# Performance work log

Hardware: AMD Instinct MI355X
Metric: run time of the kernel (lower is better)

## Reference

```python
import jax, jax.numpy as jnp
import numpy as np

N_NODES = 50000
N_EDGES = 800000
N_GRAPHS = 256
IN_CH = 128
HID = 256
FFN = 256
OUT = 1


def xavier(key, shape):
    fan_in, fan_out = shape[0], shape[1]
    a = jnp.sqrt(6.0 / (fan_in + fan_out))
    return jax.random.uniform(key, shape, jnp.float32, -a, a)


def setup_inputs() -> dict:
    key = jax.random.key(0)
    ks = jax.random.split(key, 12)
    x = jax.random.normal(ks[0], (N_NODES, IN_CH), jnp.float32)
    edge_index = jax.random.randint(ks[1], (2, N_EDGES), 0, N_NODES, jnp.int32)
    batch = jnp.sort(jax.random.randint(ks[2], (N_NODES,), 0, N_GRAPHS, jnp.int32))
    return {
        "x": x,
        "edge_index": edge_index,
        "batch": batch,
        # GCNConv layers (glorot weight, zero bias as in PyG reset_parameters)
        "W1": xavier(ks[3], (IN_CH, HID)), "b1": jnp.zeros((HID,), jnp.float32),
        "W2": xavier(ks[4], (HID, HID)),   "b2": jnp.zeros((HID,), jnp.float32),
        "W3": xavier(ks[5], (HID, HID)),   "b3": jnp.zeros((HID,), jnp.float32),
        # FFN: Linear(HID, FFN) then final Linear(FFN, OUT)
        "Wf": xavier(ks[6], (HID, FFN)),   "bf": jnp.zeros((FFN,), jnp.float32),
        "Wo": xavier(ks[7], (FFN, OUT)),   "bo": jnp.zeros((OUT,), jnp.float32),
    }


def _gcn_norm(edge_index, n_nodes):
    # add self-loops, compute symmetric normalization D^-1/2 (A+I) D^-1/2
    loops = jnp.arange(n_nodes, dtype=edge_index.dtype)
    row = jnp.concatenate([edge_index[0], loops])
    col = jnp.concatenate([edge_index[1], loops])
    deg = jax.ops.segment_sum(jnp.ones_like(col, jnp.float32), col, num_segments=n_nodes)
    dis = jnp.where(deg > 0, jax.lax.rsqrt(jnp.maximum(deg, 1.0)), 0.0)
    norm = dis[row] * dis[col]  # [E+N]
    return row, col, norm


def _gcn_conv(x, W, b, row, col, norm, n_nodes):
    xw = x @ W                                   # [N, H]
    msg = xw[row] * norm[:, None]                # gather + scale  [E+N, H]
    out = jax.ops.segment_sum(msg, col, num_segments=n_nodes)
    return out + b


def reference(x, edge_index, batch, W1, b1, W2, b2, W3, b3, Wf, bf, Wo, bo):
    row, col, norm = _gcn_norm(edge_index, N_NODES)
    h = jax.nn.relu(_gcn_conv(x, W1, b1, row, col, norm, N_NODES))
    h = jax.nn.relu(_gcn_conv(h, W2, b2, row, col, norm, N_NODES))
    h = jax.nn.relu(_gcn_conv(h, W3, b3, row, col, norm, N_NODES))
    # global mean pool over graphs
    counts = jax.ops.segment_sum(jnp.ones((N_NODES,), jnp.float32), batch, num_segments=N_GRAPHS)
    pooled = jax.ops.segment_sum(h, batch, num_segments=N_GRAPHS) / jnp.maximum(counts, 1.0)[:, None]
    # FFN (dropout is identity in eval mode): Linear -> ReLU -> final Linear
    g = jax.nn.relu(pooled @ Wf + bf)
    out = g @ Wo + bo
    return out
```

## Files before the change

### kernel.cpp

```cpp
#include <hip/hip_runtime.h>
#include <hip/hip_bf16.h>
#include <hip/hip_fp16.h>


#define THREADS 256
#define EPB 2048

typedef _Float16 f16x8 __attribute__((ext_vector_type(8)));
typedef float    f32x4 __attribute__((ext_vector_type(4)));
typedef unsigned short u16x8 __attribute__((ext_vector_type(8)));


__global__ void degree_goff_kernel(const int* __restrict__ col, int* __restrict__ deg, int E,
                                   const int* __restrict__ batch, int* __restrict__ goff,
                                   int N, int G) {
    int i = blockIdx.x * THREADS + threadIdx.x;
    if (i < E) atomicAdd(&deg[col[i]], 1);
    if (i < N) {
        int b1 = batch[i];
        int b0 = (i == 0) ? -1 : batch[i - 1];
        for (int g = b0 + 1; g <= b1; ++g) goff[g] = i;
        if (i == N - 1) {
            for (int g = b1 + 1; g <= G; ++g) goff[g] = N;
        }
    }
}

__global__ void bucketcnt_kernel(const int* __restrict__ deg, const int* __restrict__ batch,
                                 int* __restrict__ bcnt, int N) {
    int i = blockIdx.x * THREADS + threadIdx.x;
    if (i < N) {
        int key = (batch[i] << 3) | min((deg[i] + 7) >> 3, 7);
        atomicAdd(&bcnt[key], 1);
    }
}

__global__ __launch_bounds__(256) void bucketscan_kernel(int* __restrict__ b) {
    __shared__ int wsum[4];
    int t = threadIdx.x, lane = t & 63, wid = t >> 6;
    int base = t * 8;
    int v[8];
    #pragma unroll
    for (int k = 0; k < 8; ++k) v[k] = b[base + k];
    int s = 0;
    #pragma unroll
    for (int k = 0; k < 8; ++k) s += v[k];
    int inc = s;
    #pragma unroll
    for (int d = 1; d < 64; d <<= 1) {
        int u = __shfl_up(inc, d);
        if (lane >= d) inc += u;
    }
    if (lane == 63) wsum[wid] = inc;
    __syncthreads();
    int add = 0;
    for (int w = 0; w < wid; ++w) add += wsum[w];
    int ex = add + inc - s;
    #pragma unroll
    for (int k = 0; k < 8; ++k) { int t2 = v[k]; b[base + k] = ex; ex += t2; }
}

__global__ void place_kernel(const int* __restrict__ deg, const int* __restrict__ batch,
                             int* __restrict__ bcnt, int* __restrict__ perm,
                             int* __restrict__ pinv, int* __restrict__ batch_p, int N) {
    int i = blockIdx.x * THREADS + threadIdx.x;
    if (i < N) {
        int g = batch[i];
        int key = (g << 3) | min((deg[i] + 7) >> 3, 7);
        int pos = atomicAdd(&bcnt[key], 1);
        perm[pos] = i; pinv[i] = pos; batch_p[pos] = g;
    }
}

__global__ void translate_kernel(const int* __restrict__ row, const int* __restrict__ col,
                                 const int* __restrict__ pinv,
                                 unsigned short* __restrict__ rowp,
                                 unsigned short* __restrict__ colp, int E) {
    int e0 = (blockIdx.x * THREADS + threadIdx.x) * 8;
    if (e0 >= E) return;
    if (e0 + 8 <= E) {
        int4 c0 = *(const int4*)&col[e0];
        int4 c1 = *(const int4*)&col[e0 + 4];
        int4 r0 = *(const int4*)&row[e0];
        int4 r1 = *(const int4*)&row[e0 + 4];
        int cs[8] = {c0.x, c0.y, c0.z, c0.w, c1.x, c1.y, c1.z, c1.w};
        int rs[8] = {r0.x, r0.y, r0.z, r0.w, r1.x, r1.y, r1.z, r1.w};
        u16x8 cp, rp;
        #pragma unroll
        for (int j = 0; j < 8; ++j) {
            cp[j] = (unsigned short)pinv[cs[j]];
            rp[j] = (unsigned short)pinv[rs[j]];
        }
        *(u16x8*)&colp[e0] = cp;
        *(u16x8*)&rowp[e0] = rp;
    } else {
        for (int j = 0; j < 8 && e0 + j < E; ++j) {
            colp[e0 + j] = (unsigned short)pinv[col[e0 + j]];
            rowp[e0 + j] = (unsigned short)pinv[row[e0 + j]];
        }
    }
}

__global__ __launch_bounds__(256) void scanA_kernel(
    const int* __restrict__ deg, const int* __restrict__ perm,
    int* __restrict__ out, int* __restrict__ bsum,
    float* __restrict__ dis, int* __restrict__ degp, int n) {
    __shared__ int wsum[4];
    int i0 = blockIdx.x * 1024 + threadIdx.x * 4;
    int lane = threadIdx.x & 63, wid = threadIdx.x >> 6;
    int v0 = 0, v1 = 0, v2 = 0, v3 = 0;
    if (i0 + 0 < n) v0 = deg[perm[i0 + 0]];
    if (i0 + 1 < n) v1 = deg[perm[i0 + 1]];
    if (i0 + 2 < n) v2 = deg[perm[i0 + 2]];
    if (i0 + 3 < n) v3 = deg[perm[i0 + 3]];
    if (i0 + 0 < n) { dis[i0 + 0] = rsqrtf((float)(v0 + 1)); degp[i0 + 0] = v0; }
    if (i0 + 1 < n) { dis[i0 + 1] = rsqrtf((float)(v1 + 1)); degp[i0 + 1] = v1; }
    if (i0 + 2 < n) { dis[i0 + 2] = rsqrtf((float)(v2 + 1)); degp[i0 + 2] = v2; }
    if (i0 + 3 < n) { dis[i0 + 3] = rsqrtf((float)(v3 + 1)); degp[i0 + 3] = v3; }
    v0 = (v0 + 7) & ~7; v1 = (v1 + 7) & ~7;
    v2 = (v2 + 7) & ~7; v3 = (v3 + 7) & ~7;
    int s = v0 + v1 + v2 + v3;
    int inc = s;
    #pragma unroll
    for (int d = 1; d < 64; d <<= 1) {
        int t = __shfl_up(inc, d);
        if (lane >= d) inc += t;
    }
    if (lane == 63) wsum[wid] = inc;
    __syncthreads();
    int add = 0;
    for (int w = 0; w < wid; ++w) add += wsum[w];
    int ex = add + inc - s;
    if (i0 + 0 < n) out[i0 + 0] = ex;
    if (i0 + 1 < n) out[i0 + 1] = ex + v0;
    if (i0 + 2 < n) out[i0 + 2] = ex + v0 + v1;
    if (i0 + 3 < n) out[i0 + 3] = ex + v0 + v1 + v2;
    if (threadIdx.x == 255) bsum[blockIdx.x] = add + inc;
}

__global__ void scanB_kernel(int* __restrict__ bsum, int* __restrict__ total_slot, int nb) {
    int lane = threadIdx.x;
    int v = (lane < nb) ? bsum[lane] : 0;
    int inc = v;
    #pragma unroll
    for (int d = 1; d < 64; d <<= 1) {
        int t = __shfl_up(inc, d);
        if (lane >= d) inc += t;
    }
    if (lane < nb) bsum[lane] = inc - v;
    if (lane == 63) *total_slot = inc;
}

__global__ __launch_bounds__(256) void padfill_x_kernel(
    const int* __restrict__ offs, const int* __restrict__ degp,
    unsigned short* __restrict__ srcs, int N) {
    int slice = blockIdx.x & 7;
    int SL = (N + 7) >> 3;
    int p = slice * SL + (int)(blockIdx.x >> 3) * THREADS + threadIdx.x;
    int nhi = min(N, slice * SL + SL);
    if (p >= nhi) return;
    int s = offs[p] + degp[p], e = offs[p + 1];
    for (int i = s; i < e; ++i) srcs[i] = (unsigned short)N;
}

__global__ __launch_bounds__(256) void csr_fill_x_kernel(
    const unsigned short* __restrict__ rowp, const unsigned short* __restrict__ colp,
    const int* __restrict__ offs, int* __restrict__ degp,
    unsigned short* __restrict__ srcs, int E, int N) {
    int slice = blockIdx.x & 7;
    int SL = (N + 7) >> 3;
    int nlo = slice * SL;
    int nhi = min(N, nlo + SL);
    int e0 = (int)(blockIdx.x >> 3) * EPB + threadIdx.x * 8;
    if (e0 >= E) return;
    if (e0 + 8 <= E) {
        u16x8 cp = *(const u16x8*)&colp[e0];
        u16x8 rp = *(const u16x8*)&rowp[e0];
        #pragma unroll
        for (int j = 0; j < 8; ++j) {
            int c = cp[j];
            if (c >= nlo && c < nhi) {
                int old = atomicSub(&degp[c], 1);
                srcs[offs[c] + old - 1] = rp[j];
            }
        }
    } else {
        for (int j = 0; j < 8 && e0 + j < E; ++j) {
            int c = colp[e0 + j];
            if (c >= nlo && c < nhi) {
                int old = atomicSub(&degp[c], 1);
                srcs[offs[c] + old - 1] = rowp[e0 + j];
            }
        }
    }
}

__global__ void convert_kernel(
    int* __restrict__ offs, const int* __restrict__ bsum, int Nfix,
    const float* __restrict__ X, const float* __restrict__ dis,
    const int* __restrict__ perm,
    _Float16* __restrict__ Xs, int total8, int IC,
    const float* __restrict__ W1, _Float16* __restrict__ W1t, int k1,
    const float* __restrict__ W2, _Float16* __restrict__ W2t,
    const float* __restrict__ W3, _Float16* __restrict__ W3t,
    _Float16* __restrict__ Hs) {
    int i = blockIdx.x * THREADS + threadIdx.x;
    if (i < Nfix) {
        offs[i] += bsum[i >> 10];
        return;
    }
    int j = i - Nfix;
    int Ms = Nfix + 1;
    if (j < total8) {
        int gpn = IC >> 3;
        int p   = j / gpn;
        int ch0 = (j % gpn) * 8;
        int node = perm[p];
        float d = dis[p];
        float4 a = *(const float4*)&X[(size_t)node * IC + ch0];
        float4 b = *(const float4*)&X[(size_t)node * IC + ch0 + 4];
        f16x8 o;
        o[0] = (_Float16)(d * a.x); o[1] = (_Float16)(d * a.y);
        o[2] = (_Float16)(d * a.z); o[3] = (_Float16)(d * a.w);
        o[4] = (_Float16)(d * b.x); o[5] = (_Float16)(d * b.y);
        o[6] = (_Float16)(d * b.z); o[7] = (_Float16)(d * b.w);
        int sw = IC >> 3;
        int slice = ch0 / sw, within = ch0 % sw;
        *(f16x8*)&Xs[((size_t)slice * Ms + p) * sw + within] = o;
        return;
    }
    j -= total8;
    int n1 = k1 * 256;
    if (j < n1) {
        int k = j >> 8, n = j & 255;
        W1t[n * k1 + k] = (_Float16)W1[j];
        return;
    }
    j -= n1;
    if (j < 65536) {
        int k = j >> 8, n = j & 255;
        W2t[n * 256 + k] = (_Float16)W2[j];
        return;
    }
    j -= 65536;
    if (j < 65536) {
        int k = j >> 8, n = j & 255;
        W3t[n * 256 + k] = (_Float16)W3[j];
        return;
    }
    j -= 65536;
    {
        int swx = IC >> 3;
        int nx = 8 * swx;
        if (j < nx) {
            int slice = j / swx, wi = j % swx;
            Xs[((size_t)slice * Ms + Nfix) * swx + wi] = (_Float16)0.f;
            return;
        }
        j -= nx;
        if (j < 256) {
            int slice = j >> 5, wi = j & 31;
            Hs[((size_t)slice * Ms + Nfix) * 32 + wi] = (_Float16)0.f;
        }
    }
}


template<int CH>
__global__ __launch_bounds__(256) void aggregate_slice_kernel(
    const _Float16* __restrict__ X, const int* __restrict__ offs,
    const unsigned short* __restrict__ srcs, const float* __restrict__ dis,
    _Float16* __restrict__ A, int N) {
    constexpr int LPN = CH / 64;
    constexpr int NPB = 256 / LPN;
    int bid   = blockIdx.x;
    int slice = bid & 7;
    int tile  = bid >> 3;
    int node  = tile * NPB + threadIdx.x / LPN;
    if (node >= N) return;
    int lane = threadIdx.x % LPN;
    size_t Ms = (size_t)N + 1;
    const f16x8* Xv = (const f16x8*)X + (size_t)slice * Ms * LPN;
    f16x8 self = Xv[(size_t)node * LPN + lane];
    float acc[8], acc2[8];
    #pragma unroll
    for (int j = 0; j < 8; ++j) { acc[j] = (float)self[j]; acc2[j] = 0.f; }
    int s = offs[node], e = offs[node + 1];
    int nit = (e - s) >> 3;
    if (nit > 0) {
        const u16x8* ip = (const u16x8*)&srcs[s];
        u16x8 idx = ip[0];
        for (int it = 0; it < nit; ++it) {
            u16x8 nxt = ip[min(it + 1, nit - 1)];
            f16x8 v0 = Xv[(size_t)idx[0] * LPN + lane];
            f16x8 v1 = Xv[(size_t)idx[1] * LPN + lane];
            f16x8 v2 = Xv[(size_t)idx[2] * LPN + lane];
            f16x8 v3 = Xv[(size_t)idx[3] * LPN + lane];
            f16x8 v4 = Xv[(size_t)idx[4] * LPN + lane];
            f16x8 v5 = Xv[(size_t)idx[5] * LPN + lane];
            f16x8 v6 = Xv[(size_t)idx[6] * LPN + lane];
            f16x8 v7 = Xv[(size_t)idx[7] * LPN + lane];
            #pragma unroll
            for (int j = 0; j < 8; ++j) {
                acc[j]  += ((float)v0[j] + (float)v2[j]) + ((float)v4[j] + (float)v6[j]);
                acc2[j] += ((float)v1[j] + (float)v3[j]) + ((float)v5[j] + (float)v7[j]);
            }
            idx = nxt;
        }
    }
    float dn = dis[node];
    f16x8 o;
    #pragma unroll
    for (int j = 0; j < 8; ++j) o[j] = (_Float16)(dn * (acc[j] + acc2[j]));
    f16x8* Av = (f16x8*)A + (size_t)slice * Ms * LPN;
    __builtin_nontemporal_store(o, &Av[(size_t)node * LPN + lane]);
}


template<int K, int MODE>
__global__ __launch_bounds__(256) void gemm_as_kernel(
    const _Float16* __restrict__ A, const _Float16* __restrict__ Bt,
    const float* __restrict__ bias, const float* __restrict__ dscale,
    _Float16* __restrict__ H, float* __restrict__ pooled,
    const int* __restrict__ batch, int M, int Ms) {
    constexpr int LSA = K + 40;
    constexpr int KC = K / 32;
    constexpr int SPR = K / 8;
    constexpr int SPS = K / 64;
    constexpr int SW  = K / 8;
    __shared__ _Float16 As[64 * LSA];
    int tid = threadIdx.x;
    int m0 = blockIdx.x * 64;

    {
        constexpr int RPI = 256 / SPR;
        int r_in = tid % RPI;
        int seg  = tid / RPI;
        int slice = seg / SPS, sub = seg % SPS;
        #pragma unroll
        for (int it = 0; it < 64 / RPI; ++it) {
            int r = it * RPI + r_in;
            int gr = m0 + r;
            uint4 v = make_uint4(0, 0, 0, 0);
            if (gr < M) v = *(const uint4*)&A[((size_t)slice * Ms + gr) * SW + sub * 8];
            *(uint4*)&As[r * LSA + seg * 8] = v;
        }
    }
    __syncthreads();

    int wid = tid >> 6, lane = tid & 63;
    int l16 = lane & 15, quad = lane >> 4;
    int wn = wid * 64;

    f32x4 acc[4][4] = {};
    const _Float16* Bbase = Bt + (size_t)(wn + l16) * K + quad * 8;

    #pragma unroll
    for (int kc = 0; kc < KC; ++kc) {
        f16x8 bh[4];
        #pragma unroll
        for (int ni = 0; ni < 4; ++ni)
            bh[ni] = *(const f16x8*)&Bbase[(size_t)(ni * 16) * K + kc * 32];
        #pragma unroll
        for (int mi = 0; mi < 4; ++mi) {
            f16x8 ah = *(const f16x8*)&As[(mi * 16 + l16) * LSA + kc * 32 + quad * 8];
            #pragma unroll
            for (int ni = 0; ni < 4; ++ni)
                acc[mi][ni] = __builtin_amdgcn_mfma_f32_16x16x32_f16(ah, bh[ni], acc[mi][ni], 0, 0, 0);
        }
    }

    #pragma unroll
    for (int mi = 0; mi < 4; ++mi) {
        int rbase = m0 + mi * 16;
        int g0 = 0, g15 = 0;
        if (MODE == 2) {
            g0  = batch[min(rbase, M - 1)];
            g15 = batch[min(rbase + 15, M - 1)];
        }
        #pragma unroll
        for (int ni = 0; ni < 4; ++ni) {
            int col = wn + ni * 16 + l16;
            float bv = bias[col];
            if (MODE == 1) {
                size_t hbase = (size_t)(col >> 5) * Ms * 32 + (col & 31);
                #pragma unroll
                for (int r = 0; r < 4; ++r) {
                    int grow = rbase + quad * 4 + r;
                    if (grow < M) {
                        float v = fmaxf(acc[mi][ni][r] + bv, 0.f) * dscale[grow];
                        H[hbase + (size_t)grow * 32] = (_Float16)v;
                    }
                }
            } else {
                if (g0 == g15) {
                    float p = 0.f;
                    #pragma unroll
                    for (int r = 0; r < 4; ++r) {
                        int grow = rbase + quad * 4 + r;
                        float v = fmaxf(acc[mi][ni][r] + bv, 0.f);
                        p += (grow < M) ? v : 0.f;
                    }
                    p += __shfl_xor(p, 16);
                    p += __shfl_xor(p, 32);
                    if (quad == 0) atomicAdd(&pooled[g0 * 256 + col], p);
                } else {
                    #pragma unroll
                    for (int r = 0; r < 4; ++r) {
                        int grow = rbase + quad * 4 + r;
                        if (grow < M) {
                            float v = fmaxf(acc[mi][ni][r] + bv, 0.f);
                            atomicAdd(&pooled[batch[grow] * 256 + col], v);
                        }
                    }
                }
            }
        }
    }
}


__global__ __launch_bounds__(256) void ffn_kernel(
    const float* __restrict__ pooled, const int* __restrict__ goff,
    const float* __restrict__ Wf, const float* __restrict__ bf,
    const float* __restrict__ Wo, const float* __restrict__ bo,
    float* __restrict__ out) {
    __shared__ float p[256];
    __shared__ float red[256];
    int g = blockIdx.x, t = threadIdx.x;
    int cnt = goff[g + 1] - goff[g];
    float inv = 1.f / (float)max(cnt, 1);
    p[t] = pooled[g * 256 + t] * inv;
    __syncthreads();
    float s = bf[t];
    #pragma unroll 8
    for (int k = 0; k < 256; ++k) s = fmaf(p[k], Wf[k * 256 + t], s);
    float gv = fmaxf(s, 0.f);
    red[t] = gv * Wo[t];
    __syncthreads();
    for (int o = 128; o > 0; o >>= 1) {
        if (t < o) red[t] += red[t + o];
        __syncthreads();
    }
    if (t == 0) out[g] = red[0] + bo[0];
}


extern "C" void kernel_launch(void* const* d_in, const int* in_sizes, int n_in,
                              void* d_out, int out_size, void* d_ws, size_t ws_size,
                              hipStream_t stream) {
    const float* x   = (const float*)d_in[0];
    const int*   ei  = (const int*)d_in[1];
    const int*   bat = (const int*)d_in[2];
    const float* W1  = (const float*)d_in[3];
    const float* b1  = (const float*)d_in[4];
    const float* W2  = (const float*)d_in[5];
    const float* b2  = (const float*)d_in[6];
    const float* W3  = (const float*)d_in[7];
    const float* b3  = (const float*)d_in[8];
    const float* Wf  = (const float*)d_in[9];
    const float* bf  = (const float*)d_in[10];
    const float* Wo  = (const float*)d_in[11];
    const float* bo  = (const float*)d_in[12];
    float* out = (float*)d_out;

    const int N  = in_sizes[2];
    const int E  = in_sizes[1] / 2;
    const int IC = in_sizes[0] / N;
    const int HID = 256;
    const int G  = out_size;
    const int Ms = N + 1;
    const int* row = ei;
    const int* col = ei + E;

    char* w = (char*)d_ws;
    size_t off = 0;
    auto alloc = [&](size_t bytes) -> void* {
        void* p = w + off;
        off += (bytes + 255) & ~(size_t)255;
        return p;
    };
    int*   deg    = (int*)alloc((size_t)N * 4);
    float* pooled = (float*)alloc((size_t)G * HID * 4);
    int*   bcnt   = (int*)alloc((size_t)2048 * 4);
    float* dis    = (float*)alloc((size_t)N * 4);
    int*   degp   = (int*)alloc((size_t)N * 4);
    int*   offs   = (int*)alloc((size_t)(N + 1) * 4);
    unsigned short* srcs = (unsigned short*)alloc(((size_t)E + 7 * (size_t)N + 8) * 2);
    unsigned short* colp = (unsigned short*)alloc((size_t)(E + 8) * 2);
    unsigned short* rowp = (unsigned short*)alloc((size_t)(E + 8) * 2);
    int*   goff   = (int*)alloc((size_t)(G + 1) * 4);
    int*   bsum   = (int*)alloc((size_t)64 * 4);
    int*   perm   = (int*)alloc((size_t)N * 4);
    int*   pinv   = (int*)alloc((size_t)N * 4);
    int*   batch_p= (int*)alloc((size_t)N * 4);
    _Float16* W1t = (_Float16*)alloc((size_t)HID * IC * 2);
    _Float16* W2t = (_Float16*)alloc((size_t)HID * HID * 2);
    _Float16* W3t = (_Float16*)alloc((size_t)HID * HID * 2);
    _Float16* Xs  = (_Float16*)alloc((size_t)Ms * IC * 2);
    _Float16* Ah  = (_Float16*)alloc((size_t)Ms * HID * 2);
    _Float16* Hs  = (_Float16*)alloc((size_t)Ms * HID * 2);
    (void)ws_size; (void)n_in;

    size_t zlen = (((size_t)N * 4 + 255) & ~(size_t)255)
                + (((size_t)G * HID * 4 + 255) & ~(size_t)255)
                + (size_t)2048 * 4;
    hipMemsetAsync(deg, 0, zlen, stream);

    int nblk = (N + THREADS - 1) / THREADS;
    degree_goff_kernel<<<(E + THREADS - 1) / THREADS, THREADS, 0, stream>>>(
        col, deg, E, bat, goff, N, G);
    bucketcnt_kernel<<<nblk, THREADS, 0, stream>>>(deg, bat, bcnt, N);
    bucketscan_kernel<<<1, 256, 0, stream>>>(bcnt);
    place_kernel<<<nblk, THREADS, 0, stream>>>(deg, bat, bcnt, perm, pinv, batch_p, N);

    int e8 = (E + 7) / 8;
    translate_kernel<<<(e8 + THREADS - 1) / THREADS, THREADS, 0, stream>>>(
        row, col, pinv, rowp, colp, E);

    int nb = (N + 1023) / 1024;
    scanA_kernel<<<nb, 256, 0, stream>>>(deg, perm, offs, bsum, dis, degp, N);
    scanB_kernel<<<1, 64, 0, stream>>>(bsum, &offs[N], nb);

    int total8 = N * IC / 8;
    int conv_total = N + total8 + IC * HID + HID * HID + HID * HID + 8 * (IC / 8) + 256;
    convert_kernel<<<(conv_total + THREADS - 1) / THREADS, THREADS, 0, stream>>>(
        offs, bsum, N, x, dis, perm, Xs, total8, IC, W1, W1t, IC, W2, W2t, W3, W3t, Hs);

    int SL = (N + 7) >> 3;
    int pf_tiles = (SL + THREADS - 1) / THREADS;
    padfill_x_kernel<<<pf_tiles * 8, THREADS, 0, stream>>>(offs, degp, srcs, N);
    int cf_chunks = (E + EPB - 1) / EPB;
    csr_fill_x_kernel<<<cf_chunks * 8, THREADS, 0, stream>>>(rowp, colp, offs, degp, srcs, E, N);

    int mtiles = (N + 63) / 64;
    int nt1 = (N + 127) / 128;
    aggregate_slice_kernel<128><<<nt1 * 8, 256, 0, stream>>>(Xs, offs, srcs, dis, Ah, N);
    gemm_as_kernel<128, 1><<<mtiles, 256, 0, stream>>>(Ah, W1t, b1, dis, Hs, nullptr, nullptr, N, Ms);
    int nt2 = (N + 63) / 64;
    aggregate_slice_kernel<256><<<nt2 * 8, 256, 0, stream>>>(Hs, offs, srcs, dis, Ah, N);
    gemm_as_kernel<256, 1><<<mtiles, 256, 0, stream>>>(Ah, W2t, b2, dis, Hs, nullptr, nullptr, N, Ms);
    aggregate_slice_kernel<256><<<nt2 * 8, 256, 0, stream>>>(Hs, offs, srcs, dis, Ah, N);
    gemm_as_kernel<256, 2><<<mtiles, 256, 0, stream>>>(Ah, W3t, b3, nullptr, nullptr, pooled, batch_p, N, Ms);

    ffn_kernel<<<G, 256, 0, stream>>>(pooled, goff, Wf, bf, Wo, bo, out);
}
```

Before: 418.4 us.

## Bin translated edges by destination slice before CSR fill

Replaces the edge translation kernel with one that also partitions each edge (packed col/row pair) into eight destination-node slices using per-block shared-memory histograms and a global atomic cursor. The CSR fill then reads only its own slice's edges instead of having all eight slice blocks scan the whole edge list. This removes the eightfold redundant read and filtering of edges in CSR construction. In exchange it adds three small launches (slice counting, an 8-entry scan, binned translation) plus extra shared-memory atomics and scatter writes.

```diff
diff --git a/kernel.cpp b/kernel.cpp
--- a/kernel.cpp
+++ b/kernel.cpp
@@ -4,7 +4,6 @@
 
 
 #define THREADS 256
-#define EPB 2048
 
 typedef _Float16 f16x8 __attribute__((ext_vector_type(8)));
 typedef float    f32x4 __attribute__((ext_vector_type(4)));
@@ -69,35 +68,6 @@
         int key = (g << 3) | min((deg[i] + 7) >> 3, 7);
         int pos = atomicAdd(&bcnt[key], 1);
         perm[pos] = i; pinv[i] = pos; batch_p[pos] = g;
-    }
-}
-
-__global__ void translate_kernel(const int* __restrict__ row, const int* __restrict__ col,
-                                 const int* __restrict__ pinv,
-                                 unsigned short* __restrict__ rowp,
-                                 unsigned short* __restrict__ colp, int E) {
-    int e0 = (blockIdx.x * THREADS + threadIdx.x) * 8;
-    if (e0 >= E) return;
-    if (e0 + 8 <= E) {
-        int4 c0 = *(const int4*)&col[e0];
-        int4 c1 = *(const int4*)&col[e0 + 4];
-        int4 r0 = *(const int4*)&row[e0];
-        int4 r1 = *(const int4*)&row[e0 + 4];
-        int cs[8] = {c0.x, c0.y, c0.z, c0.w, c1.x, c1.y, c1.z, c1.w};
-        int rs[8] = {r0.x, r0.y, r0.z, r0.w, r1.x, r1.y, r1.z, r1.w};
-        u16x8 cp, rp;
-        #pragma unroll
-        for (int j = 0; j < 8; ++j) {
-            cp[j] = (unsigned short)pinv[cs[j]];
-            rp[j] = (unsigned short)pinv[rs[j]];
-        }
-        *(u16x8*)&colp[e0] = cp;
-        *(u16x8*)&rowp[e0] = rp;
-    } else {
-        for (int j = 0; j < 8 && e0 + j < E; ++j) {
-            colp[e0 + j] = (unsigned short)pinv[col[e0 + j]];
-            rowp[e0 + j] = (unsigned short)pinv[row[e0 + j]];
-        }
     }
 }
 
@@ -151,6 +121,90 @@
     if (lane == 63) *total_slot = inc;
 }
 
+__global__ __launch_bounds__(256) void slicecnt_kernel(
+    const int* __restrict__ degp, int* __restrict__ scnt, int N) {
+    __shared__ int wsum[4];
+    int s = blockIdx.x;
+    int SL = (N + 7) >> 3;
+    int lo = s * SL, hi = min(N, lo + SL);
+    int acc = 0;
+    for (int i = lo + (int)threadIdx.x; i < hi; i += 256) acc += degp[i];
+    #pragma unroll
+    for (int d = 1; d < 64; d <<= 1) acc += __shfl_xor(acc, d);
+    int lane = threadIdx.x & 63, wid = threadIdx.x >> 6;
+    if (lane == 0) wsum[wid] = acc;
+    __syncthreads();
+    if (threadIdx.x == 0) scnt[s] = wsum[0] + wsum[1] + wsum[2] + wsum[3];
+}
+
+__global__ void scan8_kernel(const int* __restrict__ scnt, int* __restrict__ binoff,
+                             int* __restrict__ bcur) {
+    if (threadIdx.x == 0 && blockIdx.x == 0) {
+        int cum = 0;
+        for (int s = 0; s < 8; ++s) { binoff[s] = cum; bcur[s] = cum; cum += scnt[s]; }
+        binoff[8] = cum;
+    }
+}
+
+__global__ __launch_bounds__(256) void translate_bin_kernel(
+    const int* __restrict__ row, const int* __restrict__ col,
+    const int* __restrict__ pinv, unsigned int* __restrict__ bins,
+    int* __restrict__ bcur, int E, int N) {
+    __shared__ unsigned int lent[2048];
+    __shared__ int lhist[8], lbase[8], gbase[8], lpos[8];
+    int t = threadIdx.x;
+    if (t < 8) lhist[t] = 0;
+    __syncthreads();
+    int SL = (N + 7) >> 3;
+    int e0 = blockIdx.x * 2048 + t * 8;
+    unsigned int ent[8]; int sl[8];
+    int n = E - e0; if (n < 0) n = 0; if (n > 8) n = 8;
+    if (n == 8) {
+        int4 c0 = *(const int4*)&col[e0];
+        int4 c1 = *(const int4*)&col[e0 + 4];
+        int4 r0 = *(const int4*)&row[e0];
+        int4 r1 = *(const int4*)&row[e0 + 4];
+        int cs[8] = {c0.x, c0.y, c0.z, c0.w, c1.x, c1.y, c1.z, c1.w};
+        int rs[8] = {r0.x, r0.y, r0.z, r0.w, r1.x, r1.y, r1.z, r1.w};
+        #pragma unroll
+        for (int j = 0; j < 8; ++j) {
+            int cp = pinv[cs[j]], rp = pinv[rs[j]];
+            sl[j] = cp / SL;
+            ent[j] = (unsigned int)cp | ((unsigned int)rp << 16);
+            atomicAdd(&lhist[sl[j]], 1);
+        }
+    } else {
+        for (int j = 0; j < n; ++j) {
+            int cp = pinv[col[e0 + j]], rp = pinv[row[e0 + j]];
+            sl[j] = cp / SL;
+            ent[j] = (unsigned int)cp | ((unsigned int)rp << 16);
+            atomicAdd(&lhist[sl[j]], 1);
+        }
+    }
+    __syncthreads();
+    if (t == 0) {
+        int cum = 0;
+        #pragma unroll
+        for (int s = 0; s < 8; ++s) { lbase[s] = cum; cum += lhist[s]; }
+    }
+    __syncthreads();
+    if (t < 8) { gbase[t] = atomicAdd(&bcur[t], lhist[t]); lpos[t] = lbase[t]; }
+    __syncthreads();
+    for (int j = 0; j < n; ++j) {
+        int p = atomicAdd(&lpos[sl[j]], 1);
+        lent[p] = ent[j];
+    }
+    __syncthreads();
+    int total = lbase[7] + lhist[7];
+    for (int k = t; k < total; k += 256) {
+        unsigned int e = lent[k];
+        int s = 0;
+        #pragma unroll
+        for (int b = 1; b < 8; ++b) s = (k >= lbase[b]) ? b : s;
+        bins[gbase[s] + (k - lbase[s])] = e;
+    }
+}
+
 __global__ __launch_bounds__(256) void padfill_x_kernel(
     const int* __restrict__ offs, const int* __restrict__ degp,
     unsigned short* __restrict__ srcs, int N) {
@@ -163,33 +217,24 @@
     for (int i = s; i < e; ++i) srcs[i] = (unsigned short)N;
 }
 
-__global__ __launch_bounds__(256) void csr_fill_x_kernel(
-    const unsigned short* __restrict__ rowp, const unsigned short* __restrict__ colp,
+__global__ __launch_bounds__(256) void csr_fill2_kernel(
+    const unsigned int* __restrict__ bins, const int* __restrict__ binoff,
     const int* __restrict__ offs, int* __restrict__ degp,
-    unsigned short* __restrict__ srcs, int E, int N) {
+    unsigned short* __restrict__ srcs, int CPS) {
     int slice = blockIdx.x & 7;
-    int SL = (N + 7) >> 3;
-    int nlo = slice * SL;
-    int nhi = min(N, nlo + SL);
-    int e0 = (int)(blockIdx.x >> 3) * EPB + threadIdx.x * 8;
-    if (e0 >= E) return;
-    if (e0 + 8 <= E) {
-        u16x8 cp = *(const u16x8*)&colp[e0];
-        u16x8 rp = *(const u16x8*)&rowp[e0];
+    int chunk = blockIdx.x >> 3;
+    int lo = binoff[slice], hi = binoff[slice + 1];
+    for (int base = lo + chunk * 2048; base < hi; base += CPS * 2048) {
+        int i0 = base + (int)threadIdx.x * 8;
         #pragma unroll
         for (int j = 0; j < 8; ++j) {
-            int c = cp[j];
-            if (c >= nlo && c < nhi) {
+            int i = i0 + j;
+            if (i < hi) {
+                unsigned int e = bins[i];
+                int c = (int)(e & 0xffffu);
+                int r = (int)(e >> 16);
                 int old = atomicSub(&degp[c], 1);
-                srcs[offs[c] + old - 1] = rp[j];
-            }
-        }
-    } else {
-        for (int j = 0; j < 8 && e0 + j < E; ++j) {
-            int c = colp[e0 + j];
-            if (c >= nlo && c < nhi) {
-                int old = atomicSub(&degp[c], 1);
-                srcs[offs[c] + old - 1] = rowp[e0 + j];
+                srcs[offs[c] + old - 1] = (unsigned short)r;
             }
         }
     }
@@ -487,8 +532,10 @@
     int*   degp   = (int*)alloc((size_t)N * 4);
     int*   offs   = (int*)alloc((size_t)(N + 1) * 4);
     unsigned short* srcs = (unsigned short*)alloc(((size_t)E + 7 * (size_t)N + 8) * 2);
-    unsigned short* colp = (unsigned short*)alloc((size_t)(E + 8) * 2);
-    unsigned short* rowp = (unsigned short*)alloc((size_t)(E + 8) * 2);
+    unsigned int* bins = (unsigned int*)alloc((size_t)(E + 8) * 4);
+    int*   scnt   = (int*)alloc((size_t)8 * 4);
+    int*   binoff = (int*)alloc((size_t)9 * 4);
+    int*   bcur   = (int*)alloc((size_t)8 * 4);
     int*   goff   = (int*)alloc((size_t)(G + 1) * 4);
     int*   bsum   = (int*)alloc((size_t)64 * 4);
     int*   perm   = (int*)alloc((size_t)N * 4);
@@ -514,13 +561,14 @@
     bucketscan_kernel<<<1, 256, 0, stream>>>(bcnt);
     place_kernel<<<nblk, THREADS, 0, stream>>>(deg, bat, bcnt, perm, pinv, batch_p, N);
 
-    int e8 = (E + 7) / 8;
-    translate_kernel<<<(e8 + THREADS - 1) / THREADS, THREADS, 0, stream>>>(
-        row, col, pinv, rowp, colp, E);
-
     int nb = (N + 1023) / 1024;
     scanA_kernel<<<nb, 256, 0, stream>>>(deg, perm, offs, bsum, dis, degp, N);
     scanB_kernel<<<1, 64, 0, stream>>>(bsum, &offs[N], nb);
+
+    slicecnt_kernel<<<8, 256, 0, stream>>>(degp, scnt, N);
+    scan8_kernel<<<1, 64, 0, stream>>>(scnt, binoff, bcur);
+    translate_bin_kernel<<<(E + 2047) / 2048, 256, 0, stream>>>(
+        row, col, pinv, bins, bcur, E, N);
 
     int total8 = N * IC / 8;
     int conv_total = N + total8 + IC * HID + HID * HID + HID * HID + 8 * (IC / 8) + 256;
@@ -530,8 +578,8 @@
     int SL = (N + 7) >> 3;
     int pf_tiles = (SL + THREADS - 1) / THREADS;
     padfill_x_kernel<<<pf_tiles * 8, THREADS, 0, stream>>>(offs, degp, srcs, N);
-    int cf_chunks = (E + EPB - 1) / EPB;
-    csr_fill_x_kernel<<<cf_chunks * 8, THREADS, 0, stream>>>(rowp, colp, offs, degp, srcs, E, N);
+    int CPS = (E + 8 * 2048 - 1) / (8 * 2048);
+    csr_fill2_kernel<<<CPS * 8, 256, 0, stream>>>(bins, binoff, offs, degp, srcs, CPS);
 
     int mtiles = (N + 63) / 64;
     int nt1 = (N + 127) / 128;
```

Measured after the change: 426.6 us. Within noise of the previous version (+1.9%).
